# Kernel optimization log

Hardware: AMD Instinct MI355X
Metric: run time of the kernel (lower is better)

Reference implementation:

```python
import jax, jax.numpy as jnp
import numpy as np

VOCAB = 50000
D = 200
N_CONCEPTS = 100000
B = 256
L = 8


def setup_inputs() -> dict:
    key = jax.random.key(0)
    k1, k2, k3 = jax.random.split(key, 3)
    mention_word_ids = jax.random.randint(k1, (B, L), 0, VOCAB)
    word_embedding = jax.random.normal(k2, (VOCAB, D), dtype=jnp.float32)
    dict_embedding = jax.random.normal(k3, (N_CONCEPTS, D), dtype=jnp.float32)
    return {
        "mention_word_ids": mention_word_ids,
        "word_embedding": word_embedding,
        "dict_embedding": dict_embedding,
    }


def reference(mention_word_ids, word_embedding, dict_embedding):
    # Embedding lookup [B, L, D] then mean-pool over tokens (avg_pool2d over L) -> [B, D]
    mention_rep = jnp.mean(word_embedding[mention_word_ids], axis=1)
    # Cosine similarity: dot / (||m|| * ||c||), denominator clamped at 1e-8
    m_norm = jnp.linalg.norm(mention_rep, axis=1, keepdims=True)        # [B, 1]
    c_norm = jnp.linalg.norm(dict_embedding, axis=1, keepdims=True)     # [N, 1]
    denom = jnp.maximum(m_norm * c_norm.T, 1e-8)                        # [B, N]
    sims = jnp.matmul(mention_rep, dict_embedding.T) / denom            # [B, N]
    values = jnp.max(sims, axis=1)
    indices = jnp.argmax(sims, axis=1)
    return values, indices
```

## Files before the change

### kernel.cpp

```cpp
#include <hip/hip_runtime.h>
#include <math.h>

#define BB 256
#define LL 8
#define DD 200
#define NN 100000
#define BN 32
#define NTILE (NN / BN)
#define NGRAN 28
#define GRID_SIM 512
#define NCAND 6

typedef __attribute__((ext_vector_type(8))) __bf16 bf16x8;
typedef __attribute__((ext_vector_type(16))) float f32x16;

__device__ __forceinline__ unsigned f2bf(float x) {
  unsigned u = __float_as_uint(x);
  u = (u + 0x7fffu + ((u >> 16) & 1u)) >> 16;
  return u;
}
__device__ __forceinline__ unsigned pk(float a, float b) {
  return f2bf(a) | (f2bf(b) << 16);
}
__device__ __forceinline__ bool better(float a, int ia, float b, int ib) {
  return (a > b) || (a == b && ia < ib);
}
__device__ __forceinline__ float dot4(float4 f) {
  return f.x * f.x + f.y * f.y + f.z * f.z + f.w * f.w;
}

__global__ __launch_bounds__(256) void prep_kernel(
    const int* __restrict__ ids, const float* __restrict__ we,
    float* __restrict__ repf, unsigned short* __restrict__ abf,
    float* __restrict__ mnorm) {
  int m = blockIdx.x, d = threadIdx.x;
  __shared__ float red[4];
  float r = 0.f;
  if (d < DD) {
    int base = m * LL;
#pragma unroll
    for (int l2 = 0; l2 < LL; ++l2) r += we[(size_t)ids[base + l2] * DD + d];
    r *= 0.125f;
    repf[m * DD + d] = r;
  }
  if (d < NGRAN * 8) {
    int g = d >> 3, wo = d & 7;
    abf[(g * 256 + m) * 8 + wo] = (unsigned short)f2bf(d < DD ? r : 0.f);
  }
  float sq = (d < DD) ? r * r : 0.f;
#pragma unroll
  for (int off = 32; off; off >>= 1) sq += __shfl_down(sq, off);
  if ((threadIdx.x & 63) == 0) red[threadIdx.x >> 6] = sq;
  __syncthreads();
  if (threadIdx.x == 0) mnorm[m] = sqrtf(red[0] + red[1] + red[2] + red[3]);
}

__global__ __launch_bounds__(512) void sim_kernel(
    const float* __restrict__ dict, const uint4* __restrict__ abfT,
    float4* __restrict__ partial) {
  __shared__ uint4 Bs[2][NGRAN * BN];

  int tid = threadIdx.x;
  int w = tid >> 6, l = tid & 63;
  int ln = l & 31, kh = l >> 5;
  int m = w * 32 + ln;

  uint4 areg[14];
#pragma unroll
  for (int j = 0; j < 14; ++j) areg[j] = abfT[(2 * j + kh) * 256 + m];
#pragma unroll
  for (int j = 0; j < 14; ++j)
    asm volatile("" : "+v"(areg[j].x), "+v"(areg[j].y),
                      "+v"(areg[j].z), "+v"(areg[j].w));

  int row = tid >> 4, part = tid & 15;
  const bool extra = (part < 2);
  int g0i = part >> 1, h = part & 1;

  if (tid < 192) {
    int buf = tid / 96, u = tid % 96;
    int g = 25 + u / 32, r = u & 31;
    Bs[buf][g * 32 + (r ^ (g & 7))] = make_uint4(0, 0, 0, 0);
  }

  float v1 = -INFINITY, v2 = -INFINITY;
  int i1 = 0x7fffffff, i2 = 0x7fffffff;

  int t0 = blockIdx.x;
  {
    const float* src = dict + (size_t)(t0 * BN + row) * DD;
    float4 f0 = *(const float4*)(src + 4 * part);
    float4 f1 = *(const float4*)(src + 64 + 4 * part);
    float4 f2 = *(const float4*)(src + 128 + 4 * part);
    float4 f3 = extra ? *(const float4*)(src + 192 + 4 * part)
                      : make_float4(0.f, 0.f, 0.f, 0.f);
    float sq = dot4(f0) + dot4(f1) + dot4(f2) + dot4(f3);
    sq += __shfl_xor(sq, 1); sq += __shfl_xor(sq, 2);
    sq += __shfl_xor(sq, 4); sq += __shfl_xor(sq, 8);
    float rs = 1.0f / fmaxf(sqrtf(sq), 1e-8f);
    uint2* B2 = (uint2*)&Bs[0][0];
    B2[(g0i * 32 + (row ^ (g0i & 7))) * 2 + h] =
        make_uint2(pk(f0.x * rs, f0.y * rs), pk(f0.z * rs, f0.w * rs));
    int ga = 8 + g0i;
    B2[(ga * 32 + (row ^ (ga & 7))) * 2 + h] =
        make_uint2(pk(f1.x * rs, f1.y * rs), pk(f1.z * rs, f1.w * rs));
    int gb = 16 + g0i;
    B2[(gb * 32 + (row ^ (gb & 7))) * 2 + h] =
        make_uint2(pk(f2.x * rs, f2.y * rs), pk(f2.z * rs, f2.w * rs));
    if (extra)
      B2[(24 * 32 + row) * 2 + part] =
          make_uint2(pk(f3.x * rs, f3.y * rs), pk(f3.z * rs, f3.w * rs));
  }
  __syncthreads();

  int cur = 0;
  for (int t = t0; t < NTILE; t += GRID_SIM) {
    bool hn = (t + GRID_SIM) < NTILE;
    float4 f0, f1, f2, f3;
    if (hn) {
      const float* src = dict + (size_t)((t + GRID_SIM) * BN + row) * DD;
      f0 = *(const float4*)(src + 4 * part);
      f1 = *(const float4*)(src + 64 + 4 * part);
      f2 = *(const float4*)(src + 128 + 4 * part);
      f3 = extra ? *(const float4*)(src + 192 + 4 * part)
                 : make_float4(0.f, 0.f, 0.f, 0.f);
    }
    __builtin_amdgcn_sched_barrier(0);

    f32x16 acc;
#pragma unroll
    for (int i = 0; i < 16; ++i) acc[i] = 0.f;
    const uint4* B = Bs[cur];
#pragma unroll
    for (int j = 0; j < 14; ++j) {
      int g = 2 * j + kh;
      bf16x8 a = __builtin_bit_cast(bf16x8, B[g * 32 + (ln ^ (g & 7))]);
      acc = __builtin_amdgcn_mfma_f32_32x32x16_bf16(
          a, __builtin_bit_cast(bf16x8, areg[j]), acc, 0, 0, 0);
    }

    int n0 = t * BN + 4 * kh;
#pragma unroll
    for (int r = 0; r < 16; ++r) {
      int n = n0 + (r & 3) + 8 * (r >> 2);
      float v = acc[r];
      if (v > v1) { v2 = v1; i2 = i1; v1 = v; i1 = n; }
      else if (v > v2) { v2 = v; i2 = n; }
    }

    if (hn) {
      float sq = dot4(f0) + dot4(f1) + dot4(f2) + dot4(f3);
      sq += __shfl_xor(sq, 1); sq += __shfl_xor(sq, 2);
      sq += __shfl_xor(sq, 4); sq += __shfl_xor(sq, 8);
      float rs = 1.0f / fmaxf(sqrtf(sq), 1e-8f);
      uint2* B2 = (uint2*)&Bs[cur ^ 1][0];
      B2[(g0i * 32 + (row ^ (g0i & 7))) * 2 + h] =
          make_uint2(pk(f0.x * rs, f0.y * rs), pk(f0.z * rs, f0.w * rs));
      int ga = 8 + g0i;
      B2[(ga * 32 + (row ^ (ga & 7))) * 2 + h] =
          make_uint2(pk(f1.x * rs, f1.y * rs), pk(f1.z * rs, f1.w * rs));
      int gb = 16 + g0i;
      B2[(gb * 32 + (row ^ (gb & 7))) * 2 + h] =
          make_uint2(pk(f2.x * rs, f2.y * rs), pk(f2.z * rs, f2.w * rs));
      if (extra)
        B2[(24 * 32 + row) * 2 + part] =
            make_uint2(pk(f3.x * rs, f3.y * rs), pk(f3.z * rs, f3.w * rs));
    }
    __syncthreads();
    cur ^= 1;
  }

  float w1 = __shfl_xor(v1, 32); int j1 = __shfl_xor(i1, 32);
  float w2 = __shfl_xor(v2, 32); int j2 = __shfl_xor(i2, 32);
  float o1, o2; int oi1, oi2;
  if (better(w1, j1, v1, i1)) {
    bool tt = better(v1, i1, w2, j2);
    o1 = w1; oi1 = j1; o2 = tt ? v1 : w2; oi2 = tt ? i1 : j2;
  } else {
    bool tt = better(w1, j1, v2, i2);
    o1 = v1; oi1 = i1; o2 = tt ? w1 : v2; oi2 = tt ? j1 : i2;
  }
  if (kh == 0)
    partial[(size_t)m * GRID_SIM + blockIdx.x] =
        make_float4(o1, __int_as_float(oi1), o2, __int_as_float(oi2));
}

__global__ __launch_bounds__(256) void final_kernel(
    const float* __restrict__ dict, const float* __restrict__ repf,
    const float* __restrict__ mnorm, const float4* __restrict__ partial,
    float* __restrict__ out) {
  int m = blockIdx.x, tid = threadIdx.x;
  __shared__ float repL[DD];
  __shared__ int seln[NCAND];
  __shared__ float wv[4]; __shared__ int wi[4];
  __shared__ float finv[NCAND]; __shared__ int finn[NCAND];
  if (tid < DD) repL[tid] = repf[m * DD + tid];
  __syncthreads();

  const float4* pm = partial + (size_t)m * GRID_SIM;
  float cv1[2], cv2[2]; int ci1[2], ci2[2];
#pragma unroll
  for (int e = 0; e < 2; ++e) {
    float4 E = pm[tid + e * 256];
    cv1[e] = E.x; ci1[e] = __float_as_int(E.y);
    cv2[e] = E.z; ci2[e] = __float_as_int(E.w);
  }

  for (int r = 0; r < NCAND; ++r) {
    float bv = -INFINITY; int bi = 0x7fffffff;
#pragma unroll
    for (int e = 0; e < 2; ++e) {
      bool ex1 = false, ex2 = false;
      for (int j = 0; j < r; ++j) {
        int s = seln[j];
        ex1 |= (s == ci1[e]); ex2 |= (s == ci2[e]);
      }
      if (!ex1 && better(cv1[e], ci1[e], bv, bi)) { bv = cv1[e]; bi = ci1[e]; }
      if (!ex2 && better(cv2[e], ci2[e], bv, bi)) { bv = cv2[e]; bi = ci2[e]; }
    }
#pragma unroll
    for (int off = 1; off < 64; off <<= 1) {
      float ov = __shfl_xor(bv, off); int oi = __shfl_xor(bi, off);
      if (better(ov, oi, bv, bi)) { bv = ov; bi = oi; }
    }
    if ((tid & 63) == 0) { wv[tid >> 6] = bv; wi[tid >> 6] = bi; }
    __syncthreads();
    if (tid == 0) {
      float Bv = wv[0]; int Bi = wi[0];
#pragma unroll
      for (int q = 1; q < 4; ++q)
        if (better(wv[q], wi[q], Bv, Bi)) { Bv = wv[q]; Bi = wi[q]; }
      seln[r] = Bi;
    }
    __syncthreads();
  }

  int g = tid >> 5, lane = tid & 31;
  int n = (g < NCAND) ? seln[g] : -1;
  float s1 = 0.f, s2 = 0.f;
  if (n >= 0) {
    for (int d = lane; d < DD; d += 32) {
      float b = dict[(size_t)n * DD + d];
      s1 += repL[d] * b; s2 += b * b;
    }
  }
#pragma unroll
  for (int off = 1; off < 32; off <<= 1) {
    s1 += __shfl_xor(s1, off); s2 += __shfl_xor(s2, off);
  }
  if (lane == 0 && g < NCAND) {
    finv[g] = (n >= 0) ? s1 / fmaxf(mnorm[m] * sqrtf(s2), 1e-8f) : -INFINITY;
    finn[g] = n;
  }
  __syncthreads();
  if (tid == 0) {
    float Bv = finv[0]; int Bi = finn[0];
#pragma unroll
    for (int q = 1; q < NCAND; ++q)
      if (better(finv[q], finn[q], Bv, Bi)) { Bv = finv[q]; Bi = finn[q]; }
    out[m] = Bv;
    out[BB + m] = (float)Bi;
  }
}

extern "C" void kernel_launch(void* const* d_in, const int* in_sizes, int n_in,
                              void* d_out, int out_size, void* d_ws, size_t ws_size,
                              hipStream_t stream) {
  const int* ids = (const int*)d_in[0];
  const float* we = (const float*)d_in[1];
  const float* dict = (const float*)d_in[2];
  float* out = (float*)d_out;

  char* ws = (char*)d_ws;
  unsigned short* abf = (unsigned short*)ws;
  float* repf  = (float*)(ws + 114688);
  float* mnorm = (float*)(ws + 319488);
  float4* partial = (float4*)(ws + 320512);

  prep_kernel<<<BB, 256, 0, stream>>>(ids, we, repf, abf, mnorm);
  sim_kernel<<<GRID_SIM, 512, 0, stream>>>(dict, (const uint4*)abf, partial);
  final_kernel<<<BB, 256, 0, stream>>>(dict, repf, mnorm, partial, out);
}
```

Before: 45.92 us.

## Launch one sim block per dictionary tile instead of a persistent double-buffered loop

Replaces the persistent 512-block sim kernel, which looped over tiles with an LDS double buffer and register prefetch, with a grid of 3125 blocks that each handle a single 32-row tile. The final kernel now rereads the per-tile partial top-2 candidates from global memory on every candidate round rather than holding them in registers. This removes the loop and its synchronisation, but every block reloads the 14 A-operand registers and pays launch and prologue costs. The partial buffer is about six times larger, so the final kernel reads much more data, repeated across six rounds.

```diff
diff --git a/kernel.cpp b/kernel.cpp
--- a/kernel.cpp
+++ b/kernel.cpp
@@ -8,7 +8,6 @@
 #define BN 32
 #define NTILE (NN / BN)
 #define NGRAN 28
-#define GRID_SIM 512
 #define NCAND 6
 
 typedef __attribute__((ext_vector_type(8))) __bf16 bf16x8;
@@ -58,12 +57,23 @@
 __global__ __launch_bounds__(512) void sim_kernel(
     const float* __restrict__ dict, const uint4* __restrict__ abfT,
     float4* __restrict__ partial) {
-  __shared__ uint4 Bs[2][NGRAN * BN];
-
+  __shared__ uint4 Bs[NGRAN * BN];
   int tid = threadIdx.x;
   int w = tid >> 6, l = tid & 63;
   int ln = l & 31, kh = l >> 5;
   int m = w * 32 + ln;
+  int tile = blockIdx.x;
+
+  int row = tid >> 4, part = tid & 15;
+  const bool extra = (part < 2);
+  int g0i = part >> 1, h = part & 1;
+
+  const float* src = dict + (size_t)(tile * BN + row) * DD;
+  float4 f0 = *(const float4*)(src + 4 * part);
+  float4 f1 = *(const float4*)(src + 64 + 4 * part);
+  float4 f2 = *(const float4*)(src + 128 + 4 * part);
+  float4 f3 = extra ? *(const float4*)(src + 192 + 4 * part)
+                    : make_float4(0.f, 0.f, 0.f, 0.f);
 
   uint4 areg[14];
 #pragma unroll
@@ -73,32 +83,17 @@
     asm volatile("" : "+v"(areg[j].x), "+v"(areg[j].y),
                       "+v"(areg[j].z), "+v"(areg[j].w));
 
-  int row = tid >> 4, part = tid & 15;
-  const bool extra = (part < 2);
-  int g0i = part >> 1, h = part & 1;
-
-  if (tid < 192) {
-    int buf = tid / 96, u = tid % 96;
-    int g = 25 + u / 32, r = u & 31;
-    Bs[buf][g * 32 + (r ^ (g & 7))] = make_uint4(0, 0, 0, 0);
-  }
-
-  float v1 = -INFINITY, v2 = -INFINITY;
-  int i1 = 0x7fffffff, i2 = 0x7fffffff;
-
-  int t0 = blockIdx.x;
+  if (tid < 96) {
+    int g = 25 + tid / 32, r = tid & 31;
+    Bs[g * 32 + (r ^ (g & 7))] = make_uint4(0, 0, 0, 0);
+  }
+
   {
-    const float* src = dict + (size_t)(t0 * BN + row) * DD;
-    float4 f0 = *(const float4*)(src + 4 * part);
-    float4 f1 = *(const float4*)(src + 64 + 4 * part);
-    float4 f2 = *(const float4*)(src + 128 + 4 * part);
-    float4 f3 = extra ? *(const float4*)(src + 192 + 4 * part)
-                      : make_float4(0.f, 0.f, 0.f, 0.f);
     float sq = dot4(f0) + dot4(f1) + dot4(f2) + dot4(f3);
     sq += __shfl_xor(sq, 1); sq += __shfl_xor(sq, 2);
     sq += __shfl_xor(sq, 4); sq += __shfl_xor(sq, 8);
     float rs = 1.0f / fmaxf(sqrtf(sq), 1e-8f);
-    uint2* B2 = (uint2*)&Bs[0][0];
+    uint2* B2 = (uint2*)&Bs[0];
     B2[(g0i * 32 + (row ^ (g0i & 7))) * 2 + h] =
         make_uint2(pk(f0.x * rs, f0.y * rs), pk(f0.z * rs, f0.w * rs));
     int ga = 8 + g0i;
@@ -113,63 +108,27 @@
   }
   __syncthreads();
 
-  int cur = 0;
-  for (int t = t0; t < NTILE; t += GRID_SIM) {
-    bool hn = (t + GRID_SIM) < NTILE;
-    float4 f0, f1, f2, f3;
-    if (hn) {
-      const float* src = dict + (size_t)((t + GRID_SIM) * BN + row) * DD;
-      f0 = *(const float4*)(src + 4 * part);
-      f1 = *(const float4*)(src + 64 + 4 * part);
-      f2 = *(const float4*)(src + 128 + 4 * part);
-      f3 = extra ? *(const float4*)(src + 192 + 4 * part)
-                 : make_float4(0.f, 0.f, 0.f, 0.f);
-    }
-    __builtin_amdgcn_sched_barrier(0);
-
-    f32x16 acc;
-#pragma unroll
-    for (int i = 0; i < 16; ++i) acc[i] = 0.f;
-    const uint4* B = Bs[cur];
-#pragma unroll
-    for (int j = 0; j < 14; ++j) {
-      int g = 2 * j + kh;
-      bf16x8 a = __builtin_bit_cast(bf16x8, B[g * 32 + (ln ^ (g & 7))]);
-      acc = __builtin_amdgcn_mfma_f32_32x32x16_bf16(
-          a, __builtin_bit_cast(bf16x8, areg[j]), acc, 0, 0, 0);
-    }
-
-    int n0 = t * BN + 4 * kh;
-#pragma unroll
-    for (int r = 0; r < 16; ++r) {
-      int n = n0 + (r & 3) + 8 * (r >> 2);
-      float v = acc[r];
-      if (v > v1) { v2 = v1; i2 = i1; v1 = v; i1 = n; }
-      else if (v > v2) { v2 = v; i2 = n; }
-    }
-
-    if (hn) {
-      float sq = dot4(f0) + dot4(f1) + dot4(f2) + dot4(f3);
-      sq += __shfl_xor(sq, 1); sq += __shfl_xor(sq, 2);
-      sq += __shfl_xor(sq, 4); sq += __shfl_xor(sq, 8);
-      float rs = 1.0f / fmaxf(sqrtf(sq), 1e-8f);
-      uint2* B2 = (uint2*)&Bs[cur ^ 1][0];
-      B2[(g0i * 32 + (row ^ (g0i & 7))) * 2 + h] =
-          make_uint2(pk(f0.x * rs, f0.y * rs), pk(f0.z * rs, f0.w * rs));
-      int ga = 8 + g0i;
-      B2[(ga * 32 + (row ^ (ga & 7))) * 2 + h] =
-          make_uint2(pk(f1.x * rs, f1.y * rs), pk(f1.z * rs, f1.w * rs));
-      int gb = 16 + g0i;
-      B2[(gb * 32 + (row ^ (gb & 7))) * 2 + h] =
-          make_uint2(pk(f2.x * rs, f2.y * rs), pk(f2.z * rs, f2.w * rs));
-      if (extra)
-        B2[(24 * 32 + row) * 2 + part] =
-            make_uint2(pk(f3.x * rs, f3.y * rs), pk(f3.z * rs, f3.w * rs));
-    }
-    __syncthreads();
-    cur ^= 1;
-  }
-
+  f32x16 acc;
+#pragma unroll
+  for (int i = 0; i < 16; ++i) acc[i] = 0.f;
+#pragma unroll
+  for (int j = 0; j < 14; ++j) {
+    int g = 2 * j + kh;
+    bf16x8 a = __builtin_bit_cast(bf16x8, Bs[g * 32 + (ln ^ (g & 7))]);
+    acc = __builtin_amdgcn_mfma_f32_32x32x16_bf16(
+        a, __builtin_bit_cast(bf16x8, areg[j]), acc, 0, 0, 0);
+  }
+
+  float v1 = -INFINITY, v2 = -INFINITY;
+  int i1 = 0x7fffffff, i2 = 0x7fffffff;
+  int n0 = tile * BN + 4 * kh;
+#pragma unroll
+  for (int r = 0; r < 16; ++r) {
+    int n = n0 + (r & 3) + 8 * (r >> 2);
+    float v = acc[r];
+    if (v > v1) { v2 = v1; i2 = i1; v1 = v; i1 = n; }
+    else if (v > v2) { v2 = v; i2 = n; }
+  }
   float w1 = __shfl_xor(v1, 32); int j1 = __shfl_xor(i1, 32);
   float w2 = __shfl_xor(v2, 32); int j2 = __shfl_xor(i2, 32);
   float o1, o2; int oi1, oi2;
@@ -181,7 +140,7 @@
     o1 = v1; oi1 = i1; o2 = tt ? w1 : v2; oi2 = tt ? j1 : i2;
   }
   if (kh == 0)
-    partial[(size_t)m * GRID_SIM + blockIdx.x] =
+    partial[(size_t)m * NTILE + tile] =
         make_float4(o1, __int_as_float(oi1), o2, __int_as_float(oi2));
 }
 
@@ -197,26 +156,24 @@
   if (tid < DD) repL[tid] = repf[m * DD + tid];
   __syncthreads();
 
-  const float4* pm = partial + (size_t)m * GRID_SIM;
-  float cv1[2], cv2[2]; int ci1[2], ci2[2];
-#pragma unroll
-  for (int e = 0; e < 2; ++e) {
-    float4 E = pm[tid + e * 256];
-    cv1[e] = E.x; ci1[e] = __float_as_int(E.y);
-    cv2[e] = E.z; ci2[e] = __float_as_int(E.w);
-  }
-
+  const float4* pm = partial + (size_t)m * NTILE;
   for (int r = 0; r < NCAND; ++r) {
     float bv = -INFINITY; int bi = 0x7fffffff;
 #pragma unroll
-    for (int e = 0; e < 2; ++e) {
-      bool ex1 = false, ex2 = false;
-      for (int j = 0; j < r; ++j) {
-        int s = seln[j];
-        ex1 |= (s == ci1[e]); ex2 |= (s == ci2[e]);
+    for (int e = 0; e < 13; ++e) {
+      int idx = tid + e * 256;
+      if (idx < NTILE) {
+        float4 E = pm[idx];
+        float a1 = E.x; int c1 = __float_as_int(E.y);
+        float a2 = E.z; int c2 = __float_as_int(E.w);
+        bool ex1 = false, ex2 = false;
+        for (int j = 0; j < r; ++j) {
+          int s = seln[j];
+          ex1 |= (s == c1); ex2 |= (s == c2);
+        }
+        if (!ex1 && better(a1, c1, bv, bi)) { bv = a1; bi = c1; }
+        if (!ex2 && better(a2, c2, bv, bi)) { bv = a2; bi = c2; }
       }
-      if (!ex1 && better(cv1[e], ci1[e], bv, bi)) { bv = cv1[e]; bi = ci1[e]; }
-      if (!ex2 && better(cv2[e], ci2[e], bv, bi)) { bv = cv2[e]; bi = ci2[e]; }
     }
 #pragma unroll
     for (int off = 1; off < 64; off <<= 1) {
@@ -278,6 +235,6 @@
   float4* partial = (float4*)(ws + 320512);
 
   prep_kernel<<<BB, 256, 0, stream>>>(ids, we, repf, abf, mnorm);
-  sim_kernel<<<GRID_SIM, 512, 0, stream>>>(dict, (const uint4*)abf, partial);
+  sim_kernel<<<NTILE, 512, 0, stream>>>(dict, (const uint4*)abf, partial);
   final_kernel<<<BB, 256, 0, stream>>>(dict, repf, mnorm, partial, out);
 }
```

Result: slower. 71.82 us (+56.4%).

## Stream dict tiles into LDS via async global_load_lds and convert from LDS

Applied to the files above, without the earlier changes.

Replaces the register-staged prefetch of the next dictionary tile with direct global-to-LDS async loads into a double-buffered raw fp32 staging area. Each iteration then reads the current raw tile from LDS, computes the norm, converts it to bf16 into a single-buffered operand tile, and runs the MFMA. The aim is to free VGPRs and let the memory loads overlap compute without register pressure. In exchange it adds an extra barrier per tile, roughly 50KB of extra LDS that may reduce occupancy, and puts the conversion work on the critical path before the MFMAs.

```diff
diff --git a/kernel.cpp b/kernel.cpp
--- a/kernel.cpp
+++ b/kernel.cpp
@@ -8,6 +8,7 @@
 #define BN 32
 #define NTILE (NN / BN)
 #define NGRAN 28
+#define RAWU 1600
 #define GRID_SIM 512
 #define NCAND 6
 
@@ -27,6 +28,11 @@
 }
 __device__ __forceinline__ float dot4(float4 f) {
   return f.x * f.x + f.y * f.y + f.z * f.z + f.w * f.w;
+}
+__device__ __forceinline__ void glds16(const void* g, void* l) {
+  __builtin_amdgcn_global_load_lds(
+      (const __attribute__((address_space(1))) unsigned int*)g,
+      (__attribute__((address_space(3))) unsigned int*)l, 16, 0, 0);
 }
 
 __global__ __launch_bounds__(256) void prep_kernel(
@@ -58,7 +64,8 @@
 __global__ __launch_bounds__(512) void sim_kernel(
     const float* __restrict__ dict, const uint4* __restrict__ abfT,
     float4* __restrict__ partial) {
-  __shared__ uint4 Bs[2][NGRAN * BN];
+  __shared__ uint4 Raw[2][RAWU];
+  __shared__ uint4 Bsb[NGRAN * BN];
 
   int tid = threadIdx.x;
   int w = tid >> 6, l = tid & 63;
@@ -68,73 +75,83 @@
   uint4 areg[14];
 #pragma unroll
   for (int j = 0; j < 14; ++j) areg[j] = abfT[(2 * j + kh) * 256 + m];
-#pragma unroll
-  for (int j = 0; j < 14; ++j)
-    asm volatile("" : "+v"(areg[j].x), "+v"(areg[j].y),
-                      "+v"(areg[j].z), "+v"(areg[j].w));
-
-  int row = tid >> 4, part = tid & 15;
-  const bool extra = (part < 2);
-  int g0i = part >> 1, h = part & 1;
-
-  if (tid < 192) {
-    int buf = tid / 96, u = tid % 96;
-    int g = 25 + u / 32, r = u & 31;
-    Bs[buf][g * 32 + (r ^ (g & 7))] = make_uint4(0, 0, 0, 0);
-  }
+
+  if (tid < 96) {
+    int g = 25 + tid / 32, r = tid & 31;
+    Bsb[g * 32 + (r ^ (g & 7))] = make_uint4(0, 0, 0, 0);
+  }
+
+  int row = tid >> 4, p = tid & 15;
+  const bool two = (p < 9);
 
   float v1 = -INFINITY, v2 = -INFINITY;
   int i1 = 0x7fffffff, i2 = 0x7fffffff;
 
   int t0 = blockIdx.x;
   {
-    const float* src = dict + (size_t)(t0 * BN + row) * DD;
-    float4 f0 = *(const float4*)(src + 4 * part);
-    float4 f1 = *(const float4*)(src + 64 + 4 * part);
-    float4 f2 = *(const float4*)(src + 128 + 4 * part);
-    float4 f3 = extra ? *(const float4*)(src + 192 + 4 * part)
-                      : make_float4(0.f, 0.f, 0.f, 0.f);
-    float sq = dot4(f0) + dot4(f1) + dot4(f2) + dot4(f3);
-    sq += __shfl_xor(sq, 1); sq += __shfl_xor(sq, 2);
-    sq += __shfl_xor(sq, 4); sq += __shfl_xor(sq, 8);
-    float rs = 1.0f / fmaxf(sqrtf(sq), 1e-8f);
-    uint2* B2 = (uint2*)&Bs[0][0];
-    B2[(g0i * 32 + (row ^ (g0i & 7))) * 2 + h] =
-        make_uint2(pk(f0.x * rs, f0.y * rs), pk(f0.z * rs, f0.w * rs));
-    int ga = 8 + g0i;
-    B2[(ga * 32 + (row ^ (ga & 7))) * 2 + h] =
-        make_uint2(pk(f1.x * rs, f1.y * rs), pk(f1.z * rs, f1.w * rs));
-    int gb = 16 + g0i;
-    B2[(gb * 32 + (row ^ (gb & 7))) * 2 + h] =
-        make_uint2(pk(f2.x * rs, f2.y * rs), pk(f2.z * rs, f2.w * rs));
-    if (extra)
-      B2[(24 * 32 + row) * 2 + part] =
-          make_uint2(pk(f3.x * rs, f3.y * rs), pk(f3.z * rs, f3.w * rs));
-  }
+    const char* src = (const char*)dict + (size_t)t0 * 25600;
+#pragma unroll
+    for (int i = 0; i < 3; ++i) {
+      int u0 = i * 512 + w * 64;
+      glds16(src + (u0 + l) * 16, (char*)&Raw[0][0] + u0 * 16);
+    }
+    if (w == 0) glds16(src + (1536 + l) * 16, (char*)&Raw[0][0] + 1536 * 16);
+  }
+  asm volatile("s_waitcnt vmcnt(0)" ::: "memory");
+  __builtin_amdgcn_sched_barrier(0);
   __syncthreads();
 
   int cur = 0;
   for (int t = t0; t < NTILE; t += GRID_SIM) {
     bool hn = (t + GRID_SIM) < NTILE;
-    float4 f0, f1, f2, f3;
     if (hn) {
-      const float* src = dict + (size_t)((t + GRID_SIM) * BN + row) * DD;
-      f0 = *(const float4*)(src + 4 * part);
-      f1 = *(const float4*)(src + 64 + 4 * part);
-      f2 = *(const float4*)(src + 128 + 4 * part);
-      f3 = extra ? *(const float4*)(src + 192 + 4 * part)
-                 : make_float4(0.f, 0.f, 0.f, 0.f);
-    }
-    __builtin_amdgcn_sched_barrier(0);
+      const char* src = (const char*)dict + (size_t)(t + GRID_SIM) * 25600;
+      char* dst = (char*)&Raw[cur ^ 1][0];
+#pragma unroll
+      for (int i = 0; i < 3; ++i) {
+        int u0 = i * 512 + w * 64;
+        glds16(src + (u0 + l) * 16, dst + u0 * 16);
+      }
+      if (w == 0) glds16(src + (1536 + l) * 16, dst + 1536 * 16);
+    }
+
+    {
+      const float* rrow = (const float*)&Raw[cur][0] + row * 200;
+      float4 a0 = *(const float4*)(rrow + p * 8);
+      float4 a1 = *(const float4*)(rrow + p * 8 + 4);
+      float4 b0 = make_float4(0.f, 0.f, 0.f, 0.f), b1 = b0;
+      if (two) {
+        b0 = *(const float4*)(rrow + 128 + p * 8);
+        b1 = *(const float4*)(rrow + 128 + p * 8 + 4);
+      }
+      float sq = dot4(a0) + dot4(a1) + dot4(b0) + dot4(b1);
+      sq += __shfl_xor(sq, 1); sq += __shfl_xor(sq, 2);
+      sq += __shfl_xor(sq, 4); sq += __shfl_xor(sq, 8);
+      float rs = 1.0f / fmaxf(sqrtf(sq), 1e-8f);
+      Bsb[p * 32 + (row ^ (p & 7))] =
+          make_uint4(pk(a0.x * rs, a0.y * rs), pk(a0.z * rs, a0.w * rs),
+                     pk(a1.x * rs, a1.y * rs), pk(a1.z * rs, a1.w * rs));
+      if (two) {
+        int g = 16 + p;
+        Bsb[g * 32 + (row ^ (g & 7))] =
+            make_uint4(pk(b0.x * rs, b0.y * rs), pk(b0.z * rs, b0.w * rs),
+                       pk(b1.x * rs, b1.y * rs), pk(b1.z * rs, b1.w * rs));
+      }
+    }
+    __syncthreads();
+
+#pragma unroll
+    for (int j = 0; j < 14; ++j)
+      asm volatile("" : "+v"(areg[j].x), "+v"(areg[j].y),
+                        "+v"(areg[j].z), "+v"(areg[j].w));
 
     f32x16 acc;
 #pragma unroll
     for (int i = 0; i < 16; ++i) acc[i] = 0.f;
-    const uint4* B = Bs[cur];
 #pragma unroll
     for (int j = 0; j < 14; ++j) {
       int g = 2 * j + kh;
-      bf16x8 a = __builtin_bit_cast(bf16x8, B[g * 32 + (ln ^ (g & 7))]);
+      bf16x8 a = __builtin_bit_cast(bf16x8, Bsb[g * 32 + (ln ^ (g & 7))]);
       acc = __builtin_amdgcn_mfma_f32_32x32x16_bf16(
           a, __builtin_bit_cast(bf16x8, areg[j]), acc, 0, 0, 0);
     }
@@ -149,24 +166,10 @@
     }
 
     if (hn) {
-      float sq = dot4(f0) + dot4(f1) + dot4(f2) + dot4(f3);
-      sq += __shfl_xor(sq, 1); sq += __shfl_xor(sq, 2);
-      sq += __shfl_xor(sq, 4); sq += __shfl_xor(sq, 8);
-      float rs = 1.0f / fmaxf(sqrtf(sq), 1e-8f);
-      uint2* B2 = (uint2*)&Bs[cur ^ 1][0];
-      B2[(g0i * 32 + (row ^ (g0i & 7))) * 2 + h] =
-          make_uint2(pk(f0.x * rs, f0.y * rs), pk(f0.z * rs, f0.w * rs));
-      int ga = 8 + g0i;
-      B2[(ga * 32 + (row ^ (ga & 7))) * 2 + h] =
-          make_uint2(pk(f1.x * rs, f1.y * rs), pk(f1.z * rs, f1.w * rs));
-      int gb = 16 + g0i;
-      B2[(gb * 32 + (row ^ (gb & 7))) * 2 + h] =
-          make_uint2(pk(f2.x * rs, f2.y * rs), pk(f2.z * rs, f2.w * rs));
-      if (extra)
-        B2[(24 * 32 + row) * 2 + part] =
-            make_uint2(pk(f3.x * rs, f3.y * rs), pk(f3.z * rs, f3.w * rs));
-    }
-    __syncthreads();
+      asm volatile("s_waitcnt vmcnt(0)" ::: "memory");
+      __builtin_amdgcn_sched_barrier(0);
+      __syncthreads();
+    }
     cur ^= 1;
   }
 
```

New measurement: 56.54 us. +23.1%, slower.
